# Kernel tuning notes

Hardware: AMD Instinct MI355X
Metric: run time of the kernel (lower is better)

Reference implementation:

```python
import jax, jax.numpy as jnp
import numpy as np

D_MODEL = 1024
NUM_HEADS = 16
D_K = D_MODEL // NUM_HEADS


def setup_inputs() -> dict:
    key = jax.random.key(0)
    ks = jax.random.split(key, 6)
    B, S = 2, 2048
    scale = 1.0 / np.sqrt(D_MODEL)
    x = jax.random.normal(ks[0], (B, S, D_MODEL), dtype=jnp.float32)
    w_q = jax.random.normal(ks[1], (D_MODEL, D_MODEL), dtype=jnp.float32) * scale
    w_k = jax.random.normal(ks[2], (D_MODEL, D_MODEL), dtype=jnp.float32) * scale
    w_v = jax.random.normal(ks[3], (D_MODEL, D_MODEL), dtype=jnp.float32) * scale
    w_o = jax.random.normal(ks[4], (D_MODEL, D_MODEL), dtype=jnp.float32) * scale
    b_o = jax.random.normal(ks[5], (D_MODEL,), dtype=jnp.float32) * 0.01
    return {"x": x, "w_q": w_q, "w_k": w_k, "w_v": w_v, "w_o": w_o, "b_o": b_o}


def reference(x, w_q, w_k, w_v, w_o, b_o):
    B, S, _ = x.shape
    # Linear(d, d, bias=False): y = x @ W.T ; weights stored torch-style [out, in]
    def proj(w):
        y = jnp.einsum('bsd,ed->bse', x, w)
        return y.reshape(B, S, NUM_HEADS, D_K).transpose(0, 2, 1, 3)  # [B,H,S,Dk]
    Q, K, V = proj(w_q), proj(w_k), proj(w_v)
    scores = jnp.einsum('bhqd,bhkd->bhqk', Q, K) / np.sqrt(D_K)
    attn = jax.nn.softmax(scores, axis=-1)  # dropout p=0 (eval) -> identity
    out = jnp.einsum('bhqk,bhkd->bhqd', attn, V)
    out = out.transpose(0, 2, 1, 3).reshape(B, S, D_MODEL)
    return jnp.einsum('bsd,ed->bse', out, w_o) + b_o
```

## Files before the change

### kernel.cpp

```cpp
#include <hip/hip_runtime.h>
#include <hip/hip_bf16.h>


typedef __bf16 bf16x8 __attribute__((ext_vector_type(8)));
typedef float f32x4 __attribute__((ext_vector_type(4)));
typedef float f32x16 __attribute__((ext_vector_type(16)));

__device__ __forceinline__ unsigned short f2bf(float f) {
  union { float f; unsigned int u; } c; c.f = f;
  unsigned int u = c.u;
  return (unsigned short)((u + 0x7FFFu + ((u >> 16) & 1u)) >> 16);
}

__device__ __forceinline__ unsigned int pk2bf(float a, float b) {
  union { float f; unsigned int u; } x, y;
  x.f = a; y.f = b;
  return __builtin_amdgcn_perm(y.u + 0x8000u, x.u + 0x8000u, 0x07060302u);
}

__device__ __forceinline__ bf16x8 ld_frag(const unsigned short* p) {
  union { uint4 u; bf16x8 b; } c;
  c.u = *(const uint4*)p;
  return c.b;
}

__device__ __forceinline__ uint4 cvt8(const float* __restrict__ p) {
  float4 a = *(const float4*)p;
  float4 b = *(const float4*)(p + 4);
  union { uint4 u; unsigned short s[8]; } r;
  r.s[0] = f2bf(a.x); r.s[1] = f2bf(a.y); r.s[2] = f2bf(a.z); r.s[3] = f2bf(a.w);
  r.s[4] = f2bf(b.x); r.s[5] = f2bf(b.y); r.s[6] = f2bf(b.z); r.s[7] = f2bf(b.w);
  return r.u;
}

typedef __attribute__((address_space(1))) const unsigned int as1_u32;
typedef __attribute__((address_space(3))) unsigned int as3_u32;
__device__ __forceinline__ void async16(const unsigned short* g,
                                        unsigned short* l) {
  __builtin_amdgcn_global_load_lds(
      (as1_u32*)(unsigned long long)g,
      (as3_u32*)(unsigned int)(unsigned long long)l, 16, 0, 0);
}

__global__ __launch_bounds__(256) void cvt_all(
    const float* __restrict__ s0, const float* __restrict__ s1,
    const float* __restrict__ s2, const float* __restrict__ s3,
    const float* __restrict__ s4,
    unsigned short* __restrict__ d0, unsigned short* __restrict__ d1,
    unsigned short* __restrict__ d2, unsigned short* __restrict__ d3,
    unsigned short* __restrict__ d4) {
  const float* srcs[5] = {s0, s1, s2, s3, s4};
  unsigned short* dsts[5] = {d0, d1, d2, d3, d4};
  const int ns[5] = {4194304, 1048576, 1048576, 1048576, 1048576};
  const int y = blockIdx.y;
  const int idx = (blockIdx.x * 256 + threadIdx.x) * 8;
  if (idx >= ns[y]) return;
  *(uint4*)(dsts[y] + idx) = cvt8(srcs[y] + idx);
}

template <int BM, bool OUT_F32>
__global__ __launch_bounds__(256) void gemm_bt(
    const unsigned short* __restrict__ A,
    const unsigned short* __restrict__ w0,
    const unsigned short* __restrict__ w1,
    const unsigned short* __restrict__ w2,
    const float* __restrict__ bias,
    void* __restrict__ outraw, float z0scale) {
  constexpr int NT = (BM == 128) ? 4 : 2;
  const int z = blockIdx.z;
  const unsigned short* W = (z == 0) ? w0 : ((z == 1) ? w1 : w2);
  const float scl = (z == 0) ? z0scale : 1.0f;

  __shared__ unsigned short a_lds[BM * 32];
  __shared__ unsigned short b_lds[128 * 32];

  const int tid = threadIdx.x;
  const int wave = tid >> 6, lane = tid & 63;
  const int quad = lane >> 4, l16 = lane & 15;
  const int wm = (BM == 128) ? (wave >> 1) * 64 : 0;
  const int wn = (BM == 128) ? (wave & 1) * 64 : wave * 32;
  const int bm = blockIdx.y * BM, bn = blockIdx.x * 128;

  const int rl = lane >> 2;
  const int kc = (lane & 3) ^ (rl & 3) ^ ((rl >> 2) & 3);
  const int arow = (BM == 128) ? (wave * 32 + rl) : (wave * 16 + rl);
  const unsigned short* ga = A + (size_t)(bm + arow) * 1024 + kc * 8;
  const unsigned short* gb = W + (size_t)(bn + wave * 32 + rl) * 1024 + kc * 8;
  unsigned short* la = &a_lds[((BM == 128) ? wave * 32 : wave * 16) * 32];
  unsigned short* lb = &b_lds[wave * 32 * 32];

  const int rsw8 = ((l16 & 3) ^ ((l16 >> 2) & 3)) * 8;

  f32x4 acc[4][NT] = {};

  for (int k0 = 0; k0 < 1024; k0 += 32) {
    async16(ga, la);
    if (BM == 128) async16(ga + 16 * 1024, la + 16 * 32);
    async16(gb, lb);
    async16(gb + 16 * 1024, lb + 16 * 32);
    ga += 32; gb += 32;
    __syncthreads();

    bf16x8 af[4], bfr[NT];
#pragma unroll
    for (int t = 0; t < 4; ++t)
      af[t] = ld_frag(&a_lds[(wm + t * 16 + l16) * 32 + ((quad * 8) ^ rsw8)]);
#pragma unroll
    for (int t = 0; t < NT; ++t)
      bfr[t] = ld_frag(&b_lds[(wn + t * 16 + l16) * 32 + ((quad * 8) ^ rsw8)]);
#pragma unroll
    for (int mt = 0; mt < 4; ++mt)
#pragma unroll
      for (int nt = 0; nt < NT; ++nt)
        acc[mt][nt] = __builtin_amdgcn_mfma_f32_16x16x32_bf16(
            af[mt], bfr[nt], acc[mt][nt], 0, 0, 0);
    __syncthreads();
  }

#pragma unroll
  for (int nt = 0; nt < NT; ++nt) {
    const int n = bn + wn + nt * 16 + l16;
    const float bv = bias ? bias[n] : 0.0f;
#pragma unroll
    for (int mt = 0; mt < 4; ++mt)
#pragma unroll
      for (int r = 0; r < 4; ++r) {
        const int m = bm + wm + mt * 16 + quad * 4 + r;
        const float v = acc[mt][nt][r] * scl + bv;
        if (OUT_F32)
          ((float*)outraw)[(size_t)z * 4096 * 1024 + (size_t)m * 1024 + n] = v;
        else
          ((unsigned short*)outraw)[(size_t)z * 4096 * 1024 +
                                    (size_t)m * 1024 + n] = f2bf(v);
      }
  }
}

__global__ __launch_bounds__(256) void transpose_v(
    const unsigned short* __restrict__ v, unsigned short* __restrict__ vt) {
  const int st0 = blockIdx.x * 64;
  const int bh = blockIdx.y, b = bh >> 4, h = bh & 15;
  __shared__ unsigned short t[64 * 72];
  const int tid = threadIdx.x;
#pragma unroll
  for (int it = 0; it < 2; ++it) {
    const int c = it * 256 + tid;
    const int row = c >> 3, c8 = (c & 7) * 8;
    *(uint4*)&t[row * 72 + c8] =
        *(const uint4*)(v + (size_t)(b * 2048 + st0 + row) * 1024 + h * 64 + c8);
  }
  __syncthreads();
#pragma unroll
  for (int it = 0; it < 2; ++it) {
    const int c = it * 256 + tid;
    const int drow = c >> 3, s8 = (c & 7) * 8;
    union { uint4 u; unsigned short e[8]; } o;
#pragma unroll
    for (int j = 0; j < 8; ++j) o.e[j] = t[(s8 + j) * 72 + drow];
    *(uint4*)(vt + ((size_t)bh * 64 + drow) * 2048 + st0 + s8) = o.u;
  }
}

__global__ __launch_bounds__(256, 4) void attn4(
    const unsigned short* __restrict__ qkv,
    const unsigned short* __restrict__ vt_g,
    unsigned short* __restrict__ ab) {
  constexpr size_t PL = (size_t)4096 * 1024;
  const int qt = blockIdx.x, bh = blockIdx.y;
  const int b = bh >> 4, h = bh & 15;

  __shared__ __align__(16) unsigned short kvs[2][2][64 * 64];
  __shared__ float sm_l[2][2][32];

  const int tid = threadIdx.x;
  const int wave = tid >> 6, lane = tid & 63;
  const int ws = wave >> 1, wq = wave & 1;
  const int hi = lane >> 5, l32 = lane & 31;
  const int row8 = lane >> 3;
  const int sl = (lane & 7) ^ (row8 & 7);
  const int swz = (l32 & 7) * 8;

  const unsigned short* qrow =
      qkv + (size_t)(b * 2048 + qt * 64 + wq * 32 + l32) * 1024 + h * 64 +
      hi * 8;
  bf16x8 qf[4];
#pragma unroll
  for (int kc = 0; kc < 4; ++kc) qf[kc] = ld_frag(qrow + kc * 16);

  const unsigned short* gK =
      qkv + PL + (size_t)(b * 2048 + ws * 1024 + wq * 32 + row8) * 1024 +
      h * 64 + sl * 8;
  const unsigned short* gV =
      vt_g + (size_t)bh * 64 * 2048 + (size_t)(wq * 32 + row8) * 2048 +
      ws * 1024 + sl * 8;
  unsigned short* lK = &kvs[ws][0][wq * 4 * 512];
  unsigned short* lV = &kvs[ws][1][wq * 4 * 512];

  f32x16 o_acc[2] = {};
  float l_part = 0.0f;

  for (int t = 0; t < 16; ++t) {
#pragma unroll
    for (int c = 0; c < 4; ++c) {
      async16(gK + (size_t)c * 8 * 1024, lK + c * 512);
      async16(gV + (size_t)c * 8 * 2048, lV + c * 512);
    }
    gK += 64 * 1024;
    gV += 64;
    __syncthreads();

    f32x16 st[2] = {};
#pragma unroll
    for (int mb = 0; mb < 2; ++mb)
#pragma unroll
      for (int kc = 0; kc < 4; ++kc) {
        bf16x8 ak = ld_frag(
            &kvs[ws][0][(mb * 32 + l32) * 64 + (((2 * kc + hi) * 8) ^ swz)]);
        st[mb] = __builtin_amdgcn_mfma_f32_32x32x16_bf16(ak, qf[kc], st[mb],
                                                         0, 0, 0);
      }

    unsigned int u[2][4][2];
#pragma unroll
    for (int mb = 0; mb < 2; ++mb) {
#pragma unroll
      for (int r = 0; r < 16; ++r) {
        const float p = __builtin_amdgcn_exp2f(st[mb][r]);
        st[mb][r] = p;
        l_part += p;
      }
#pragma unroll
      for (int g = 0; g < 4; ++g) {
        u[mb][g][0] = pk2bf(st[mb][g * 4 + 0], st[mb][g * 4 + 1]);
        u[mb][g][1] = pk2bf(st[mb][g * 4 + 2], st[mb][g * 4 + 3]);
      }
    }

#pragma unroll
    for (int ks = 0; ks < 4; ++ks) {
      const int m = ks >> 1, g = (ks & 1) * 2;
      unsigned int a0 = u[m][g][0], b0 = u[m][g + 1][0];
      unsigned int a1 = u[m][g][1], b1 = u[m][g + 1][1];
      asm("v_permlane32_swap_b32 %0, %1" : "+v"(a0), "+v"(b0));
      asm("v_permlane32_swap_b32 %0, %1" : "+v"(a1), "+v"(b1));
      union { unsigned int w[4]; bf16x8 f; } pa;
      pa.w[0] = a0; pa.w[1] = a1; pa.w[2] = b0; pa.w[3] = b1;
#pragma unroll
      for (int nb = 0; nb < 2; ++nb) {
        bf16x8 bv = ld_frag(
            &kvs[ws][1][(nb * 32 + l32) * 64 + (((2 * ks + hi) * 8) ^ swz)]);
        o_acc[nb] = __builtin_amdgcn_mfma_f32_32x32x16_bf16(pa.f, bv,
                                                            o_acc[nb], 0, 0, 0);
      }
    }
    __syncthreads();
  }

  float lsum = l_part + __shfl_xor(l_part, 32);

  float* sm_o = (float*)&kvs[0][0][0];
  if (ws == 1) {
#pragma unroll
    for (int nb = 0; nb < 2; ++nb)
#pragma unroll
      for (int r = 0; r < 16; ++r) {
        const int q = (r & 3) + 8 * (r >> 2) + 4 * hi;
        sm_o[wq * 2048 + q * 64 + nb * 32 + l32] = o_acc[nb][r];
      }
  }
  if (lane < 32) sm_l[ws][wq][l32] = lsum;
  __syncthreads();

  if (ws == 0) {
#pragma unroll
    for (int r = 0; r < 16; ++r) {
      const int q = (r & 3) + 8 * (r >> 2) + 4 * hi;
      const float inv = 1.0f / (sm_l[0][wq][q] + sm_l[1][wq][q]);
      const size_t row = (size_t)(b * 2048 + qt * 64 + wq * 32 + q);
#pragma unroll
      for (int nb = 0; nb < 2; ++nb) {
        const float v =
            (o_acc[nb][r] + sm_o[wq * 2048 + q * 64 + nb * 32 + l32]) * inv;
        ab[row * 1024 + h * 64 + nb * 32 + l32] = f2bf(v);
      }
    }
  }
}

extern "C" void kernel_launch(void* const* d_in, const int* in_sizes, int n_in,
                              void* d_out, int out_size, void* d_ws,
                              size_t ws_size, hipStream_t stream) {
  const float* x  = (const float*)d_in[0];
  const float* wq = (const float*)d_in[1];
  const float* wk = (const float*)d_in[2];
  const float* wv = (const float*)d_in[3];
  const float* wo = (const float*)d_in[4];
  const float* bo = (const float*)d_in[5];

  constexpr size_t PL = (size_t)4096 * 1024;
  unsigned short* qkv = (unsigned short*)d_ws;
  unsigned short* ab  = qkv + 2 * PL;
  unsigned short* xb  = qkv + 3 * PL;
  unsigned short* vt  = xb;
  unsigned short* wqb = qkv + 4 * PL;
  unsigned short* wkb = wqb + 1024 * 1024;
  unsigned short* wvb = wkb + 1024 * 1024;
  unsigned short* wob = wvb + 1024 * 1024;

  const float QSCALE = 0.18033688011112042f;

  cvt_all<<<dim3(2048, 5), 256, 0, stream>>>(x, wq, wk, wv, wo,
                                             xb, wqb, wkb, wvb, wob);
  gemm_bt<128, false><<<dim3(8, 32, 3), 256, 0, stream>>>(
      xb, wqb, wkb, wvb, nullptr, qkv, QSCALE);
  transpose_v<<<dim3(32, 32), 256, 0, stream>>>(qkv + 2 * PL, vt);
  attn4<<<dim3(32, 32), 256, 0, stream>>>(qkv, vt, ab);
  gemm_bt<64, true><<<dim3(8, 64, 1), 256, 0, stream>>>(
      ab, wob, wob, wob, bo, d_out, 1.0f);
}
```

Baseline: 197.4 us.

## Split attention work per wave by key half instead of query half

Each wave now handles all 64 query rows against its own 32-key slice of each tile, rather than 32 queries against all 64 keys. Each K/V fragment read from shared memory is therefore reused across two query groups, which halves LDS reads per MFMA. The cost is doubled accumulator registers (launch bounds lowered to 3 blocks per CU) and a longer multi-stage reduction across four waves at the end. It also adds s_setprio around the MFMA blocks and uses rcp in place of a division.

New measurement: 201.8 us. 1.02x slower.

```diff
diff --git a/kernel.cpp b/kernel.cpp
--- a/kernel.cpp
+++ b/kernel.cpp
@@ -161,43 +161,49 @@
   }
 }
 
-__global__ __launch_bounds__(256, 4) void attn4(
+__global__ __launch_bounds__(256, 3) void attn5(
     const unsigned short* __restrict__ qkv,
     const unsigned short* __restrict__ vt_g,
     unsigned short* __restrict__ ab) {
   constexpr size_t PL = (size_t)4096 * 1024;
   const int qt = blockIdx.x, bh = blockIdx.y;
-  const int b = bh >> 4, h = bh & 15;
+  const int b = bh >> 4, hd = bh & 15;
 
   __shared__ __align__(16) unsigned short kvs[2][2][64 * 64];
-  __shared__ float sm_l[2][2][32];
+  __shared__ float sm_l[4][2][32];
+  __shared__ float sm_lt[2][32];
 
   const int tid = threadIdx.x;
   const int wave = tid >> 6, lane = tid & 63;
-  const int ws = wave >> 1, wq = wave & 1;
+  const int ws = wave >> 1, hh = wave & 1;
   const int hi = lane >> 5, l32 = lane & 31;
   const int row8 = lane >> 3;
   const int sl = (lane & 7) ^ (row8 & 7);
   const int swz = (l32 & 7) * 8;
 
-  const unsigned short* qrow =
-      qkv + (size_t)(b * 2048 + qt * 64 + wq * 32 + l32) * 1024 + h * 64 +
-      hi * 8;
-  bf16x8 qf[4];
-#pragma unroll
-  for (int kc = 0; kc < 4; ++kc) qf[kc] = ld_frag(qrow + kc * 16);
+  bf16x8 qf[2][4];
+#pragma unroll
+  for (int qg = 0; qg < 2; ++qg) {
+    const unsigned short* qrow =
+        qkv + (size_t)(b * 2048 + qt * 64 + qg * 32 + l32) * 1024 + hd * 64 +
+        hi * 8;
+#pragma unroll
+    for (int kc = 0; kc < 4; ++kc) qf[qg][kc] = ld_frag(qrow + kc * 16);
+  }
 
   const unsigned short* gK =
-      qkv + PL + (size_t)(b * 2048 + ws * 1024 + wq * 32 + row8) * 1024 +
-      h * 64 + sl * 8;
+      qkv + PL + (size_t)(b * 2048 + ws * 1024 + hh * 32 + row8) * 1024 +
+      hd * 64 + sl * 8;
   const unsigned short* gV =
-      vt_g + (size_t)bh * 64 * 2048 + (size_t)(wq * 32 + row8) * 2048 +
+      vt_g + (size_t)bh * 64 * 2048 + (size_t)(hh * 32 + row8) * 2048 +
       ws * 1024 + sl * 8;
-  unsigned short* lK = &kvs[ws][0][wq * 4 * 512];
-  unsigned short* lV = &kvs[ws][1][wq * 4 * 512];
-
-  f32x16 o_acc[2] = {};
-  float l_part = 0.0f;
+  unsigned short* lK = &kvs[ws][0][hh * 4 * 512];
+  unsigned short* lV = &kvs[ws][1][hh * 4 * 512];
+
+  f32x16 o_acc[2][2] = {};
+  float l_part[2] = {0.0f, 0.0f};
+
+  const int krow = (hh * 32 + l32) * 64;
 
   for (int t = 0; t < 16; ++t) {
 #pragma unroll
@@ -210,80 +216,130 @@
     __syncthreads();
 
     f32x16 st[2] = {};
-#pragma unroll
-    for (int mb = 0; mb < 2; ++mb)
-#pragma unroll
-      for (int kc = 0; kc < 4; ++kc) {
-        bf16x8 ak = ld_frag(
-            &kvs[ws][0][(mb * 32 + l32) * 64 + (((2 * kc + hi) * 8) ^ swz)]);
-        st[mb] = __builtin_amdgcn_mfma_f32_32x32x16_bf16(ak, qf[kc], st[mb],
-                                                         0, 0, 0);
-      }
+    __builtin_amdgcn_s_setprio(1);
+#pragma unroll
+    for (int kc = 0; kc < 4; ++kc) {
+      bf16x8 ak = ld_frag(&kvs[ws][0][krow + (((2 * kc + hi) * 8) ^ swz)]);
+      st[0] = __builtin_amdgcn_mfma_f32_32x32x16_bf16(ak, qf[0][kc], st[0],
+                                                      0, 0, 0);
+      st[1] = __builtin_amdgcn_mfma_f32_32x32x16_bf16(ak, qf[1][kc], st[1],
+                                                      0, 0, 0);
+    }
+    __builtin_amdgcn_s_setprio(0);
 
     unsigned int u[2][4][2];
 #pragma unroll
-    for (int mb = 0; mb < 2; ++mb) {
+    for (int qg = 0; qg < 2; ++qg) {
 #pragma unroll
       for (int r = 0; r < 16; ++r) {
-        const float p = __builtin_amdgcn_exp2f(st[mb][r]);
-        st[mb][r] = p;
-        l_part += p;
+        const float p = __builtin_amdgcn_exp2f(st[qg][r]);
+        st[qg][r] = p;
+        l_part[qg] += p;
       }
 #pragma unroll
       for (int g = 0; g < 4; ++g) {
-        u[mb][g][0] = pk2bf(st[mb][g * 4 + 0], st[mb][g * 4 + 1]);
-        u[mb][g][1] = pk2bf(st[mb][g * 4 + 2], st[mb][g * 4 + 3]);
+        u[qg][g][0] = pk2bf(st[qg][g * 4 + 0], st[qg][g * 4 + 1]);
+        u[qg][g][1] = pk2bf(st[qg][g * 4 + 2], st[qg][g * 4 + 3]);
       }
     }
 
 #pragma unroll
-    for (int ks = 0; ks < 4; ++ks) {
-      const int m = ks >> 1, g = (ks & 1) * 2;
-      unsigned int a0 = u[m][g][0], b0 = u[m][g + 1][0];
-      unsigned int a1 = u[m][g][1], b1 = u[m][g + 1][1];
-      asm("v_permlane32_swap_b32 %0, %1" : "+v"(a0), "+v"(b0));
-      asm("v_permlane32_swap_b32 %0, %1" : "+v"(a1), "+v"(b1));
-      union { unsigned int w[4]; bf16x8 f; } pa;
-      pa.w[0] = a0; pa.w[1] = a1; pa.w[2] = b0; pa.w[3] = b1;
-#pragma unroll
-      for (int nb = 0; nb < 2; ++nb) {
-        bf16x8 bv = ld_frag(
-            &kvs[ws][1][(nb * 32 + l32) * 64 + (((2 * ks + hi) * 8) ^ swz)]);
-        o_acc[nb] = __builtin_amdgcn_mfma_f32_32x32x16_bf16(pa.f, bv,
-                                                            o_acc[nb], 0, 0, 0);
+    for (int ks = 0; ks < 2; ++ks) {
+      bf16x8 bv0 = ld_frag(
+          &kvs[ws][1][(0 * 32 + l32) * 64 + (((hh * 4 + ks * 2 + hi) * 8) ^ swz)]);
+      bf16x8 bv1 = ld_frag(
+          &kvs[ws][1][(1 * 32 + l32) * 64 + (((hh * 4 + ks * 2 + hi) * 8) ^ swz)]);
+#pragma unroll
+      for (int qg = 0; qg < 2; ++qg) {
+        unsigned int a0 = u[qg][2 * ks][0], b0 = u[qg][2 * ks + 1][0];
+        unsigned int a1 = u[qg][2 * ks][1], b1 = u[qg][2 * ks + 1][1];
+        asm("v_permlane32_swap_b32 %0, %1" : "+v"(a0), "+v"(b0));
+        asm("v_permlane32_swap_b32 %0, %1" : "+v"(a1), "+v"(b1));
+        union { unsigned int w[4]; bf16x8 f; } pa;
+        pa.w[0] = a0; pa.w[1] = a1; pa.w[2] = b0; pa.w[3] = b1;
+        __builtin_amdgcn_s_setprio(1);
+        o_acc[qg][0] = __builtin_amdgcn_mfma_f32_32x32x16_bf16(pa.f, bv0,
+                                                               o_acc[qg][0],
+                                                               0, 0, 0);
+        o_acc[qg][1] = __builtin_amdgcn_mfma_f32_32x32x16_bf16(pa.f, bv1,
+                                                               o_acc[qg][1],
+                                                               0, 0, 0);
+        __builtin_amdgcn_s_setprio(0);
       }
     }
     __syncthreads();
   }
 
-  float lsum = l_part + __shfl_xor(l_part, 32);
+  float lsum[2];
+#pragma unroll
+  for (int qg = 0; qg < 2; ++qg)
+    lsum[qg] = l_part[qg] + __shfl_xor(l_part[qg], 32);
+  if (lane < 32) {
+    sm_l[wave][0][l32] = lsum[0];
+    sm_l[wave][1][l32] = lsum[1];
+  }
 
   float* sm_o = (float*)&kvs[0][0][0];
-  if (ws == 1) {
-#pragma unroll
-    for (int nb = 0; nb < 2; ++nb)
+  if (wave >= 2) {
+#pragma unroll
+    for (int qg = 0; qg < 2; ++qg)
+#pragma unroll
+      for (int nb = 0; nb < 2; ++nb)
+#pragma unroll
+        for (int r = 0; r < 16; ++r) {
+          const int q = qg * 32 + (r & 3) + 8 * (r >> 2) + 4 * hi;
+          sm_o[(wave - 2) * 4096 + q * 64 + nb * 32 + l32] = o_acc[qg][nb][r];
+        }
+  }
+  __syncthreads();
+
+  if (tid < 64) {
+    const int qg = tid >> 5, qq = tid & 31;
+    sm_lt[qg][qq] = sm_l[0][qg][qq] + sm_l[1][qg][qq] + sm_l[2][qg][qq] +
+                    sm_l[3][qg][qq];
+  }
+  if (wave < 2) {
+#pragma unroll
+    for (int qg = 0; qg < 2; ++qg)
+#pragma unroll
+      for (int nb = 0; nb < 2; ++nb)
+#pragma unroll
+        for (int r = 0; r < 16; ++r) {
+          const int q = qg * 32 + (r & 3) + 8 * (r >> 2) + 4 * hi;
+          o_acc[qg][nb][r] += sm_o[wave * 4096 + q * 64 + nb * 32 + l32];
+        }
+  }
+  __syncthreads();
+
+  if (wave == 1) {
+#pragma unroll
+    for (int qg = 0; qg < 2; ++qg)
+#pragma unroll
+      for (int nb = 0; nb < 2; ++nb)
+#pragma unroll
+        for (int r = 0; r < 16; ++r) {
+          const int q = qg * 32 + (r & 3) + 8 * (r >> 2) + 4 * hi;
+          sm_o[q * 64 + nb * 32 + l32] = o_acc[qg][nb][r];
+        }
+  }
+  __syncthreads();
+
+  if (wave == 0) {
+#pragma unroll
+    for (int qg = 0; qg < 2; ++qg)
 #pragma unroll
       for (int r = 0; r < 16; ++r) {
-        const int q = (r & 3) + 8 * (r >> 2) + 4 * hi;
-        sm_o[wq * 2048 + q * 64 + nb * 32 + l32] = o_acc[nb][r];
-      }
-  }
-  if (lane < 32) sm_l[ws][wq][l32] = lsum;
-  __syncthreads();
-
-  if (ws == 0) {
-#pragma unroll
-    for (int r = 0; r < 16; ++r) {
-      const int q = (r & 3) + 8 * (r >> 2) + 4 * hi;
-      const float inv = 1.0f / (sm_l[0][wq][q] + sm_l[1][wq][q]);
-      const size_t row = (size_t)(b * 2048 + qt * 64 + wq * 32 + q);
-#pragma unroll
-      for (int nb = 0; nb < 2; ++nb) {
-        const float v =
-            (o_acc[nb][r] + sm_o[wq * 2048 + q * 64 + nb * 32 + l32]) * inv;
-        ab[row * 1024 + h * 64 + nb * 32 + l32] = f2bf(v);
-      }
-    }
+        const int crow = (r & 3) + 8 * (r >> 2) + 4 * hi;
+        const int q = qg * 32 + crow;
+        const float inv = __builtin_amdgcn_rcpf(sm_lt[qg][crow]);
+        const size_t row = (size_t)(b * 2048 + qt * 64 + q);
+#pragma unroll
+        for (int nb = 0; nb < 2; ++nb) {
+          const float v =
+              (o_acc[qg][nb][r] + sm_o[q * 64 + nb * 32 + l32]) * inv;
+          ab[row * 1024 + hd * 64 + nb * 32 + l32] = f2bf(v);
+        }
+      }
   }
 }
 
@@ -314,7 +370,7 @@
   gemm_bt<128, false><<<dim3(8, 32, 3), 256, 0, stream>>>(
       xb, wqb, wkb, wvb, nullptr, qkv, QSCALE);
   transpose_v<<<dim3(32, 32), 256, 0, stream>>>(qkv + 2 * PL, vt);
-  attn4<<<dim3(32, 32), 256, 0, stream>>>(qkv, vt, ab);
+  attn5<<<dim3(32, 32), 256, 0, stream>>>(qkv, vt, ab);
   gemm_bt<64, true><<<dim3(8, 64, 1), 256, 0, stream>>>(
       ab, wob, wob, wob, bo, d_out, 1.0f);
 }
```

## Double-buffer LDS tiles in GEMM to overlap async loads with MFMA

Applied to the files above, without the earlier changes.

The projection GEMM now uses two LDS buffers for the A and B tiles. It prefetches the next K-slice with async global-to-LDS copies while MFMAs run on the current slice, and drops one barrier per iteration. This is meant to hide global load latency behind compute. It doubles LDS use per block, which may lower occupancy, and it relies on the barrier to cover completion of the async copies.

New measurement: 196.6 us. About the same (-0.4%).

```diff
diff --git a/kernel.cpp b/kernel.cpp
--- a/kernel.cpp
+++ b/kernel.cpp
@@ -71,8 +71,8 @@
   const unsigned short* W = (z == 0) ? w0 : ((z == 1) ? w1 : w2);
   const float scl = (z == 0) ? z0scale : 1.0f;
 
-  __shared__ unsigned short a_lds[BM * 32];
-  __shared__ unsigned short b_lds[128 * 32];
+  __shared__ unsigned short a_lds[2][BM * 32];
+  __shared__ unsigned short b_lds[2][128 * 32];
 
   const int tid = threadIdx.x;
   const int wave = tid >> 6, lane = tid & 63;
@@ -86,35 +86,50 @@
   const int arow = (BM == 128) ? (wave * 32 + rl) : (wave * 16 + rl);
   const unsigned short* ga = A + (size_t)(bm + arow) * 1024 + kc * 8;
   const unsigned short* gb = W + (size_t)(bn + wave * 32 + rl) * 1024 + kc * 8;
-  unsigned short* la = &a_lds[((BM == 128) ? wave * 32 : wave * 16) * 32];
-  unsigned short* lb = &b_lds[wave * 32 * 32];
+  const int abase = ((BM == 128) ? wave * 32 : wave * 16) * 32;
+  const int bbase = wave * 32 * 32;
 
   const int rsw8 = ((l16 & 3) ^ ((l16 >> 2) & 3)) * 8;
 
   f32x4 acc[4][NT] = {};
 
+  async16(ga, &a_lds[0][abase]);
+  if (BM == 128) async16(ga + 16 * 1024, &a_lds[0][abase + 16 * 32]);
+  async16(gb, &b_lds[0][bbase]);
+  async16(gb + 16 * 1024, &b_lds[0][bbase + 16 * 32]);
+  ga += 32; gb += 32;
+  __syncthreads();
+
+  int cur = 0;
+#pragma unroll 2
   for (int k0 = 0; k0 < 1024; k0 += 32) {
-    async16(ga, la);
-    if (BM == 128) async16(ga + 16 * 1024, la + 16 * 32);
-    async16(gb, lb);
-    async16(gb + 16 * 1024, lb + 16 * 32);
-    ga += 32; gb += 32;
-    __syncthreads();
+    if (k0 < 992) {
+      const int nxt = cur ^ 1;
+      async16(ga, &a_lds[nxt][abase]);
+      if (BM == 128) async16(ga + 16 * 1024, &a_lds[nxt][abase + 16 * 32]);
+      async16(gb, &b_lds[nxt][bbase]);
+      async16(gb + 16 * 1024, &b_lds[nxt][bbase + 16 * 32]);
+      ga += 32; gb += 32;
+    }
 
     bf16x8 af[4], bfr[NT];
 #pragma unroll
     for (int t = 0; t < 4; ++t)
-      af[t] = ld_frag(&a_lds[(wm + t * 16 + l16) * 32 + ((quad * 8) ^ rsw8)]);
+      af[t] =
+          ld_frag(&a_lds[cur][(wm + t * 16 + l16) * 32 + ((quad * 8) ^ rsw8)]);
 #pragma unroll
     for (int t = 0; t < NT; ++t)
-      bfr[t] = ld_frag(&b_lds[(wn + t * 16 + l16) * 32 + ((quad * 8) ^ rsw8)]);
+      bfr[t] =
+          ld_frag(&b_lds[cur][(wn + t * 16 + l16) * 32 + ((quad * 8) ^ rsw8)]);
 #pragma unroll
     for (int mt = 0; mt < 4; ++mt)
 #pragma unroll
       for (int nt = 0; nt < NT; ++nt)
         acc[mt][nt] = __builtin_amdgcn_mfma_f32_16x16x32_bf16(
             af[mt], bfr[nt], acc[mt][nt], 0, 0, 0);
+
     __syncthreads();
+    cur ^= 1;
   }
 
 #pragma unroll
```

## Double GEMM K-tile to 64 with row-XOR LDS swizzle and swapped grid order

Applied to the files above, without the earlier changes.

The projection GEMMs now stage a K-depth of 64 per iteration instead of 32, which halves the number of barrier pairs and doubles the MFMA work between syncs. The LDS layout uses a new 8-way XOR swizzle on the row index to avoid bank conflicts at the wider stride. The grid is transposed so that consecutive blocks walk along M while sharing a weight column tile, which may improve L2 reuse of the weights. It adds a launch_bounds occupancy hint and doubles shared memory use per block, which could limit occupancy.

Result: faster. 181.3 us (-8.2%).

```diff
diff --git a/kernel.cpp b/kernel.cpp
--- a/kernel.cpp
+++ b/kernel.cpp
@@ -59,7 +59,7 @@
 }
 
 template <int BM, bool OUT_F32>
-__global__ __launch_bounds__(256) void gemm_bt(
+__global__ __launch_bounds__(256, 3) void gemm_bt(
     const unsigned short* __restrict__ A,
     const unsigned short* __restrict__ w0,
     const unsigned short* __restrict__ w1,
@@ -67,53 +67,64 @@
     const float* __restrict__ bias,
     void* __restrict__ outraw, float z0scale) {
   constexpr int NT = (BM == 128) ? 4 : 2;
+  constexpr int RA = BM / 4;
   const int z = blockIdx.z;
   const unsigned short* W = (z == 0) ? w0 : ((z == 1) ? w1 : w2);
   const float scl = (z == 0) ? z0scale : 1.0f;
 
-  __shared__ unsigned short a_lds[BM * 32];
-  __shared__ unsigned short b_lds[128 * 32];
+  __shared__ unsigned short a_lds[BM * 64];
+  __shared__ unsigned short b_lds[128 * 64];
 
   const int tid = threadIdx.x;
   const int wave = tid >> 6, lane = tid & 63;
   const int quad = lane >> 4, l16 = lane & 15;
   const int wm = (BM == 128) ? (wave >> 1) * 64 : 0;
   const int wn = (BM == 128) ? (wave & 1) * 64 : wave * 32;
-  const int bm = blockIdx.y * BM, bn = blockIdx.x * 128;
-
-  const int rl = lane >> 2;
-  const int kc = (lane & 3) ^ (rl & 3) ^ ((rl >> 2) & 3);
-  const int arow = (BM == 128) ? (wave * 32 + rl) : (wave * 16 + rl);
-  const unsigned short* ga = A + (size_t)(bm + arow) * 1024 + kc * 8;
-  const unsigned short* gb = W + (size_t)(bn + wave * 32 + rl) * 1024 + kc * 8;
-  unsigned short* la = &a_lds[((BM == 128) ? wave * 32 : wave * 16) * 32];
-  unsigned short* lb = &b_lds[wave * 32 * 32];
-
-  const int rsw8 = ((l16 & 3) ^ ((l16 >> 2) & 3)) * 8;
+  const int bm = blockIdx.x * BM, bn = blockIdx.y * 128;
+
+  const int r8 = lane >> 3;
+  const int sl = (lane & 7) ^ r8;
+  const unsigned short* ga = A + (size_t)(bm + wave * RA + r8) * 1024 + sl * 8;
+  const unsigned short* gb = W + (size_t)(bn + wave * 32 + r8) * 1024 + sl * 8;
+  unsigned short* la = &a_lds[wave * RA * 64];
+  unsigned short* lb = &b_lds[wave * 32 * 64];
 
   f32x4 acc[4][NT] = {};
 
-  for (int k0 = 0; k0 < 1024; k0 += 32) {
-    async16(ga, la);
-    if (BM == 128) async16(ga + 16 * 1024, la + 16 * 32);
-    async16(gb, lb);
-    async16(gb + 16 * 1024, lb + 16 * 32);
-    ga += 32; gb += 32;
+  for (int k0 = 0; k0 < 1024; k0 += 64) {
+#pragma unroll
+    for (int c = 0; c < RA / 8; ++c)
+      async16(ga + (size_t)c * 8 * 1024, la + c * 512);
+#pragma unroll
+    for (int c = 0; c < 4; ++c)
+      async16(gb + (size_t)c * 8 * 1024, lb + c * 512);
+    ga += 64; gb += 64;
     __syncthreads();
 
-    bf16x8 af[4], bfr[NT];
-#pragma unroll
-    for (int t = 0; t < 4; ++t)
-      af[t] = ld_frag(&a_lds[(wm + t * 16 + l16) * 32 + ((quad * 8) ^ rsw8)]);
-#pragma unroll
-    for (int t = 0; t < NT; ++t)
-      bfr[t] = ld_frag(&b_lds[(wn + t * 16 + l16) * 32 + ((quad * 8) ^ rsw8)]);
-#pragma unroll
-    for (int mt = 0; mt < 4; ++mt)
-#pragma unroll
-      for (int nt = 0; nt < NT; ++nt)
-        acc[mt][nt] = __builtin_amdgcn_mfma_f32_16x16x32_bf16(
-            af[mt], bfr[nt], acc[mt][nt], 0, 0, 0);
+    bf16x8 af[2][4], bfr[2][NT];
+#pragma unroll
+    for (int kk = 0; kk < 2; ++kk) {
+#pragma unroll
+      for (int t = 0; t < 4; ++t) {
+        const int row = wm + t * 16 + l16;
+        af[kk][t] =
+            ld_frag(&a_lds[row * 64 + (((kk * 4 + quad) ^ (row & 7)) * 8)]);
+      }
+#pragma unroll
+      for (int t = 0; t < NT; ++t) {
+        const int row = wn + t * 16 + l16;
+        bfr[kk][t] =
+            ld_frag(&b_lds[row * 64 + (((kk * 4 + quad) ^ (row & 7)) * 8)]);
+      }
+    }
+#pragma unroll
+    for (int kk = 0; kk < 2; ++kk)
+#pragma unroll
+      for (int mt = 0; mt < 4; ++mt)
+#pragma unroll
+        for (int nt = 0; nt < NT; ++nt)
+          acc[mt][nt] = __builtin_amdgcn_mfma_f32_16x16x32_bf16(
+              af[kk][mt], bfr[kk][nt], acc[mt][nt], 0, 0, 0);
     __syncthreads();
   }
 
@@ -311,10 +322,10 @@
 
   cvt_all<<<dim3(2048, 5), 256, 0, stream>>>(x, wq, wk, wv, wo,
                                              xb, wqb, wkb, wvb, wob);
-  gemm_bt<128, false><<<dim3(8, 32, 3), 256, 0, stream>>>(
+  gemm_bt<128, false><<<dim3(32, 8, 3), 256, 0, stream>>>(
       xb, wqb, wkb, wvb, nullptr, qkv, QSCALE);
   transpose_v<<<dim3(32, 32), 256, 0, stream>>>(qkv + 2 * PL, vt);
   attn4<<<dim3(32, 32), 256, 0, stream>>>(qkv, vt, ab);
-  gemm_bt<64, true><<<dim3(8, 64, 1), 256, 0, stream>>>(
+  gemm_bt<64, true><<<dim3(64, 8, 1), 256, 0, stream>>>(
       ab, wob, wob, wob, bo, d_out, 1.0f);
 }
```
